# Kernel tuning notes

Hardware: AMD Instinct MI355X
Metric: run time of the kernel (lower is better)

Reference implementation:

```python
import jax, jax.numpy as jnp
import numpy as np

NQ = 18      # num_qubits
DEPTH = 6    # variational depth
C64 = jnp.complex64


def _rx(t):
    c = jnp.cos(t / 2).astype(C64)
    s = jnp.sin(t / 2).astype(C64)
    return jnp.stack([jnp.stack([c, -1j * s]), jnp.stack([-1j * s, c])])


def _ry(t):
    c = jnp.cos(t / 2).astype(C64)
    s = jnp.sin(t / 2).astype(C64)
    return jnp.stack([jnp.stack([c, -s]), jnp.stack([s, c])])


def _rz(t):
    tc = t.astype(C64)
    z = jnp.zeros((), C64)
    return jnp.stack([jnp.stack([jnp.exp(-1j * tc / 2), z]),
                      jnp.stack([z, jnp.exp(1j * tc / 2)])])


def _apply_1q(state, U, w):
    # state: flat (2**NQ,) amplitudes, wire 0 = most-significant bit (PennyLane order)
    s = state.reshape(2 ** w, 2, -1)
    s = jnp.einsum('ab,ibj->iaj', U, s)
    return s.reshape(-1)


def _apply_cnot(state, w):
    # CNOT on adjacent wires (w, w+1): flip target amplitudes where control=1
    s = state.reshape(2 ** w, 2, 2, -1)
    s = jnp.concatenate([s[:, :1], s[:, 1:, ::-1]], axis=1)
    return s.reshape(-1)


def _simulate(params, basis):
    state = jnp.zeros(2 ** NQ, C64).at[0].set(1.0)
    # learnable basis rotation (intended: RX/RY/RZ with basis[w, 0/1/2])
    for w in range(NQ):
        state = _apply_1q(state, _rx(basis[w, 0]), w)
        state = _apply_1q(state, _ry(basis[w, 1]), w)
        state = _apply_1q(state, _rz(basis[w, 2]), w)
    for layer in range(DEPTH):
        for w in range(NQ):
            state = _apply_1q(state, _rx(params[layer, w, 0]), w)
            state = _apply_1q(state, _ry(params[layer, w, 1]), w)
            state = _apply_1q(state, _rz(params[layer, w, 2]), w)
        for w in range(NQ - 1):
            state = _apply_cnot(state, w)
    # <Z_0>: prob(wire0=0) - prob(wire0=1)
    p = jnp.abs(state.reshape(2, -1)) ** 2
    return (p[0].sum() - p[1].sum()).astype(jnp.float32)


def setup_inputs() -> dict:
    key = jax.random.key(0)
    k1, k2, k3 = jax.random.split(key, 3)
    inputs = jax.random.normal(k1, (32, 128), dtype=jnp.float32)
    params = jax.random.normal(k2, (DEPTH, NQ, 3), dtype=jnp.float32)
    basis = jax.random.normal(k3, (NQ, 3), dtype=jnp.float32)
    return {"inputs": inputs, "params": params, "basis": basis}


def reference(inputs, params, basis):
    # The original loops over batch but the circuit never consumes `inputs`,
    # so every batch element yields the same expectation value.
    e = _simulate(params, basis)
    return jnp.broadcast_to(e, (inputs.shape[0],))
```

## Files before the change

### kernel.cpp

```cpp
#include <hip/hip_runtime.h>


__device__ __forceinline__ float2 cmul(float2 a, float2 b){
  return make_float2(a.x*b.x - a.y*b.y, a.x*b.y + a.y*b.x);
}
__device__ __forceinline__ float2 cadd(float2 a, float2 b){
  return make_float2(a.x + b.x, a.y + b.y);
}
struct M2 { float2 m00, m01, m10, m11; };
__device__ __forceinline__ M2 mmul(const M2& A, const M2& B){
  M2 C;
  C.m00 = cadd(cmul(A.m00,B.m00), cmul(A.m01,B.m10));
  C.m01 = cadd(cmul(A.m00,B.m01), cmul(A.m01,B.m11));
  C.m10 = cadd(cmul(A.m10,B.m00), cmul(A.m11,B.m10));
  C.m11 = cadd(cmul(A.m10,B.m01), cmul(A.m11,B.m11));
  return C;
}
__device__ __forceinline__ M2 mrx(float t){
  float c = cosf(0.5f*t), s = sinf(0.5f*t);
  M2 R; R.m00 = make_float2(c,0.f);  R.m01 = make_float2(0.f,-s);
        R.m10 = make_float2(0.f,-s); R.m11 = make_float2(c,0.f);
  return R;
}
__device__ __forceinline__ M2 mry(float t){
  float c = cosf(0.5f*t), s = sinf(0.5f*t);
  M2 R; R.m00 = make_float2(c,0.f); R.m01 = make_float2(-s,0.f);
        R.m10 = make_float2(s,0.f); R.m11 = make_float2(c,0.f);
  return R;
}
__device__ __forceinline__ M2 mrz(float t){
  float c = cosf(0.5f*t), s = sinf(0.5f*t);
  M2 R; R.m00 = make_float2(c,-s);    R.m01 = make_float2(0.f,0.f);
        R.m10 = make_float2(0.f,0.f); R.m11 = make_float2(c,s);
  return R;
}

__global__ __launch_bounds__(64) void sim_lc(const float* __restrict__ params,
                                             const float* __restrict__ basis,
                                             float* __restrict__ out, int n){
  __shared__ float2 mats[42][4];
  const int lane = threadIdx.x;

  if (lane < 42){
    const float* p;
    if (lane < 6) p = basis + lane*3;
    else { int g = lane - 6; int l = g/6, w = g%6; p = params + (l*18 + w)*3; }
    M2 U = mmul(mrz(p[2]), mmul(mry(p[1]), mrx(p[0])));
    mats[lane][0]=U.m00; mats[lane][1]=U.m01; mats[lane][2]=U.m10; mats[lane][3]=U.m11;
  }
  __syncthreads();

  float ax = (lane == 0) ? 1.f : 0.f, ay = 0.f;

  auto gate = [&](int gi, int w){
    float2 u00 = mats[gi][0], u01 = mats[gi][1], u10 = mats[gi][2], u11 = mats[gi][3];
    const int bm = 1 << (5 - w);
    float px = __shfl_xor(ax, bm, 64);
    float py = __shfl_xor(ay, bm, 64);
    const bool hi = (lane & bm) != 0;
    float lx = hi ? px : ax, ly = hi ? py : ay;
    float hx = hi ? ax : px, hy = hi ? ay : py;
    float2 c0 = hi ? u10 : u00, c1 = hi ? u11 : u01;
    ax = c0.x*lx - c0.y*ly + c1.x*hx - c1.y*hy;
    ay = c0.x*ly + c0.y*lx + c1.x*hy + c1.y*hx;
  };

  #pragma unroll
  for (int w = 0; w < 6; ++w) gate(w, w);
  #pragma unroll
  for (int l = 0; l < 6; ++l){
    #pragma unroll
    for (int w = 0; w < 6; ++w) gate(6 + l*6 + w, w);
    #pragma unroll
    for (int w = 0; w < 5; ++w){
      int src = lane ^ (((lane >> (5 - w)) & 1) << (4 - w));
      ax = __shfl(ax, src, 64);
      ay = __shfl(ay, src, 64);
    }
  }

  float pr = ax*ax + ay*ay;
  float part = (lane & 32) ? -pr : pr;
  #pragma unroll
  for (int off = 32; off; off >>= 1) part += __shfl_xor(part, off, 64);
  if (lane < n) out[lane] = part;
}

extern "C" void kernel_launch(void* const* d_in, const int* in_sizes, int n_in,
                              void* d_out, int out_size, void* d_ws, size_t ws_size,
                              hipStream_t stream){
  (void)in_sizes; (void)n_in; (void)d_ws; (void)ws_size;
  const float* params = (const float*)d_in[1];
  const float* basis  = (const float*)d_in[2];
  float* out = (float*)d_out;
  sim_lc<<<1, 64, 0, stream>>>(params, basis, out, out_size);
}
```

Before: 61.67 us.

## Absorb CNOT permutations into lane-index basis change via compile-time masks

Instead of physically permuting amplitudes with five shuffles per layer for the CNOT ladder, the kernel tracks the linear (XOR) basis transform at compile time and rewrites each subsequent gate's partner mask and high-bit parity mask accordingly. Each gate now does one xor-shuffle pair plus a popcount parity test, and the final Z measurement uses the transformed parity mask. This removes 60 cross-lane shuffles at the cost of slightly more per-gate index arithmetic.

```diff
diff --git a/kernel.cpp b/kernel.cpp
--- a/kernel.cpp
+++ b/kernel.cpp
@@ -1,5 +1,23 @@
 #include <hip/hip_runtime.h>
 
+
+struct Masks { unsigned m[42]; unsigned r[42]; unsigned z; };
+
+constexpr Masks make_masks(){
+  Masks M{};
+  unsigned V[6], R[6];
+  for (int b = 0; b < 6; ++b){ V[b] = 1u << b; R[b] = 1u << b; }
+  int g = 0;
+  for (int w = 0; w < 6; ++w){ int b = 5 - w; M.m[g] = V[b]; M.r[g] = R[b]; ++g; }
+  for (int l = 0; l < 6; ++l){
+    for (int w = 0; w < 6; ++w){ int b = 5 - w; M.m[g] = V[b]; M.r[g] = R[b]; ++g; }
+    for (int b = 5; b >= 1; --b) V[b] ^= V[b-1];
+    for (int b = 4; b >= 0; --b) R[b] ^= R[b+1];
+  }
+  M.z = R[5];
+  return M;
+}
+constexpr Masks MK = make_masks();
 
 __device__ __forceinline__ float2 cmul(float2 a, float2 b){
   return make_float2(a.x*b.x - a.y*b.y, a.x*b.y + a.y*b.x);
@@ -52,35 +70,23 @@
 
   float ax = (lane == 0) ? 1.f : 0.f, ay = 0.f;
 
-  auto gate = [&](int gi, int w){
-    float2 u00 = mats[gi][0], u01 = mats[gi][1], u10 = mats[gi][2], u11 = mats[gi][3];
-    const int bm = 1 << (5 - w);
-    float px = __shfl_xor(ax, bm, 64);
-    float py = __shfl_xor(ay, bm, 64);
-    const bool hi = (lane & bm) != 0;
-    float lx = hi ? px : ax, ly = hi ? py : ay;
-    float hx = hi ? ax : px, hy = hi ? ay : py;
-    float2 c0 = hi ? u10 : u00, c1 = hi ? u11 : u01;
-    ax = c0.x*lx - c0.y*ly + c1.x*hx - c1.y*hy;
-    ay = c0.x*ly + c0.y*lx + c1.x*hy + c1.y*hx;
-  };
-
   #pragma unroll
-  for (int w = 0; w < 6; ++w) gate(w, w);
-  #pragma unroll
-  for (int l = 0; l < 6; ++l){
-    #pragma unroll
-    for (int w = 0; w < 6; ++w) gate(6 + l*6 + w, w);
-    #pragma unroll
-    for (int w = 0; w < 5; ++w){
-      int src = lane ^ (((lane >> (5 - w)) & 1) << (4 - w));
-      ax = __shfl(ax, src, 64);
-      ay = __shfl(ay, src, 64);
-    }
+  for (int g = 0; g < 42; ++g){
+    const int m = (int)MK.m[g];
+    const int r = (int)MK.r[g];
+    float2 u00 = mats[g][0], u01 = mats[g][1], u10 = mats[g][2], u11 = mats[g][3];
+    float px = __shfl_xor(ax, m, 64);
+    float py = __shfl_xor(ay, m, 64);
+    const bool hi = (__popc(lane & r) & 1) != 0;
+    float2 A = hi ? u11 : u00;
+    float2 B = hi ? u10 : u01;
+    float nx = A.x*ax - A.y*ay + B.x*px - B.y*py;
+    float ny = A.x*ay + A.y*ax + B.x*py + B.y*px;
+    ax = nx; ay = ny;
   }
 
   float pr = ax*ax + ay*ay;
-  float part = (lane & 32) ? -pr : pr;
+  float part = (__popc(lane & (int)MK.z) & 1) ? -pr : pr;
   #pragma unroll
   for (int off = 32; off; off >>= 1) part += __shfl_xor(part, off, 64);
   if (lane < n) out[lane] = part;
```

New measurement: 58.87 us. 4.5% less time.
